# Performance work log

Hardware: AMD Instinct MI355X
Metric: run time of the kernel (lower is better)

## Reference

```python
import jax, jax.numpy as jnp
import numpy as np

NUM_EMBEDDINGS = 1024
EMBEDDING_DIM = 64
COMMITMENT_COST = 0.25


def setup_inputs() -> dict:
    key = jax.random.key(0)
    k1, k2 = jax.random.split(key)
    inputs = jax.random.normal(k1, (32, 4096, EMBEDDING_DIM), dtype=jnp.float32)
    lim = 1.0 / NUM_EMBEDDINGS
    embedding = jax.random.uniform(k2, (NUM_EMBEDDINGS, EMBEDDING_DIM),
                                   dtype=jnp.float32, minval=-lim, maxval=lim)
    return {"inputs": inputs, "embedding": embedding}


def reference(inputs, embedding):
    input_shape = inputs.shape
    flat = inputs.reshape(-1, EMBEDDING_DIM)                     # [N, D]
    # Squared euclidean distances via the expanded form (same math as torch cdist trick)
    distances = (jnp.sum(flat ** 2, axis=1, keepdims=True)
                 + jnp.sum(embedding ** 2, axis=1)
                 - 2.0 * flat @ embedding.T)                     # [N, K]
    encoding_indices = jnp.argmin(distances, axis=1)             # [N]
    # one-hot @ embedding == gather of nearest code rows
    quantized = embedding[encoding_indices].reshape(input_shape)
    e_latent_loss = jnp.mean((jax.lax.stop_gradient(quantized) - inputs) ** 2)
    q_latent_loss = jnp.mean((quantized - jax.lax.stop_gradient(inputs)) ** 2)
    loss = q_latent_loss + COMMITMENT_COST * e_latent_loss
    # straight-through estimator
    quantized_st = inputs + jax.lax.stop_gradient(quantized - inputs)
    return loss, quantized_st, encoding_indices[:, None]
```

## Files before the change

### kernel.cpp

```cpp
#include <hip/hip_runtime.h>

#define D 64
#define K 1024
#define NROWS (32 * 4096)
#define NELEM (NROWS * D)
#define COMMIT 0.25f
#define DELTA 1.2e-4f
#define HDELTA 6e-5f
#define RPB 128
#define CHUNK 128
#define EPAD 68
#define CBYTES (CHUNK * EPAD * 2)

typedef __attribute__((ext_vector_type(8))) short short8v;
typedef __attribute__((ext_vector_type(4))) float f32x4;
typedef unsigned long long u64;

#define FORSLOT8(M) M(0) M(1) M(2) M(3) M(4) M(5) M(6) M(7)

static __device__ __forceinline__ float fence(float v) {
    asm("" : "+v"(v));
    return v;
}

static __device__ __forceinline__ unsigned short f2bf(float f) {
    unsigned u = __float_as_uint(f);
    return (unsigned short)((u + 0x7FFFu + ((u >> 16) & 1u)) >> 16);
}

static __device__ __forceinline__ float np_sumsq64(const float* __restrict__ e) {
    float r[8];
#pragma unroll
    for (int j = 0; j < 8; ++j) r[j] = fence(e[j] * e[j]);
#pragma unroll
    for (int t = 1; t < 8; ++t)
#pragma unroll
        for (int j = 0; j < 8; ++j) r[j] = r[j] + fence(e[8 * t + j] * e[8 * t + j]);
    return ((r[0] + r[1]) + (r[2] + r[3])) + ((r[4] + r[5]) + (r[6] + r[7]));
}

static __device__ __forceinline__ float exact_score(
    const float* __restrict__ xrow, const float* __restrict__ erow, float R,
    float N) {
    float a = 0.0f;
#pragma unroll
    for (int i = 0; i < D; ++i) a = __builtin_fmaf(xrow[i], erow[i], a);
    return (R + N) - 2.0f * a;
}

__global__ void prep_emb_kernel(const float* __restrict__ emb,
                                float* __restrict__ enorm,
                                unsigned short* __restrict__ e_pad,
                                float* __restrict__ loss_slot) {
    int k = blockIdx.x * blockDim.x + threadIdx.x;
    if (k == 0) *loss_slot = 0.0f;
    if (k >= K) return;
    float n = np_sumsq64(emb + k * D);
    enorm[k] = n;
    const float* e = emb + k * D;
    unsigned short* row = e_pad + k * EPAD;
#pragma unroll
    for (int i = 0; i < D; ++i) row[i] = f2bf(e[i]);
    float nh = -0.5f * n;
    unsigned nb = __float_as_uint(nh);
    row[64] = (unsigned short)(nb & 0xFFFFu);
    row[65] = (unsigned short)(nb >> 16);
    row[66] = 0;
    row[67] = 0;
}

#define GLDS(SRC, DST, SZ)                                                  \
    __builtin_amdgcn_global_load_lds(                                       \
        (const __attribute__((address_space(1))) unsigned int*)(SRC),       \
        (__attribute__((address_space(3))) unsigned int*)(DST), SZ, 0, 0)

__global__ __launch_bounds__(256, 1) void argmin_kernel(
    const float* __restrict__ x, const float* __restrict__ emb,
    const float* __restrict__ enorm, const unsigned short* __restrict__ e_pad,
    float* __restrict__ out_q, float* __restrict__ idx_f,
    float* __restrict__ loss_slot) {
    const int tid = threadIdx.x;
    const int l = tid & 63;
    const int w = tid >> 6;
    const int col = l & 15;
    const int koff = (l >> 4) * 8;
    const int blockrow = blockIdx.x * RPB;
    const int wrow = blockrow + w * 32;

    __shared__ unsigned short eB[CHUNK * EPAD];
    __shared__ int cnt[RPB];
    __shared__ int clist[RPB][4];
    __shared__ int bidx[RPB];
    __shared__ float wsum[4];

#define DECL_A(rt, h)                                                       \
    short8v Ahi_##rt##_##h;                                                 \
    { const float* p = x + (size_t)(wrow + rt * 16 + col) * D + h * 32 + koff; \
      float4 q0 = *(const float4*)p, q1 = *(const float4*)(p + 4);          \
      Ahi_##rt##_##h[0] = (short)f2bf(q0.x);                                \
      Ahi_##rt##_##h[1] = (short)f2bf(q0.y);                                \
      Ahi_##rt##_##h[2] = (short)f2bf(q0.z);                                \
      Ahi_##rt##_##h[3] = (short)f2bf(q0.w);                                \
      Ahi_##rt##_##h[4] = (short)f2bf(q1.x);                                \
      Ahi_##rt##_##h[5] = (short)f2bf(q1.y);                                \
      Ahi_##rt##_##h[6] = (short)f2bf(q1.z);                                \
      Ahi_##rt##_##h[7] = (short)f2bf(q1.w); }
    DECL_A(0, 0) DECL_A(0, 1) DECL_A(1, 0) DECL_A(1, 1)

#define SLOTROW(s) (((s) / 4) * 16 + (l >> 4) * 4 + ((s) % 4))

#define STAGE(c)                                                            \
    {                                                                       \
        const char* src = (const char*)e_pad + (size_t)(c) * CBYTES;        \
        char* dst = (char*)eB;                                              \
        _Pragma("unroll")                                                   \
        for (int i = 0; i < 4; ++i) {                                       \
            int off = w * 1024 + i * 4096;                                  \
            GLDS(src + off + l * 16, dst + off, 16);                        \
        }                                                                   \
        { int off4 = 16384 + w * 256;                                       \
          GLDS(src + off4 + l * 4, dst + off4, 4); }                        \
    }

#define DECL_MA(s) float mA_##s = -3.402823466e+38f;
    FORSLOT8(DECL_MA)
#define MFMA2A(rt, sA, sB, sC, sD)                                          \
    { f32x4 acc = {Nc, Nc, Nc, Nc};                                         \
      acc = __builtin_amdgcn_mfma_f32_16x16x32_bf16(Ahi_##rt##_0, Bhi0, acc, 0, 0, 0); \
      acc = __builtin_amdgcn_mfma_f32_16x16x32_bf16(Ahi_##rt##_1, Bhi1, acc, 0, 0, 0); \
      mA_##sA = fmaxf(mA_##sA, acc[0]);                                     \
      mA_##sB = fmaxf(mA_##sB, acc[1]);                                     \
      mA_##sC = fmaxf(mA_##sC, acc[2]);                                     \
      mA_##sD = fmaxf(mA_##sD, acc[3]); }
    for (int c = 0; c < 8; ++c) {
        __syncthreads();
        STAGE(c)
        __syncthreads();
#pragma unroll 2
        for (int nt = 0; nt < 8; ++nt) {
            const int cc = nt * 16 + col;
            const short8v Bhi0 = *(const short8v*)(&eB[cc * EPAD + koff]);
            const short8v Bhi1 = *(const short8v*)(&eB[cc * EPAD + 32 + koff]);
            const float Nc = *(const float*)(&eB[cc * EPAD + 64]);
            MFMA2A(0, 0, 1, 2, 3) MFMA2A(1, 4, 5, 6, 7)
        }
    }
#define BFA(s)                                                              \
    mA_##s = fmaxf(mA_##s, __shfl_xor(mA_##s, 1));                          \
    mA_##s = fmaxf(mA_##s, __shfl_xor(mA_##s, 2));                          \
    mA_##s = fmaxf(mA_##s, __shfl_xor(mA_##s, 4));                          \
    mA_##s = fmaxf(mA_##s, __shfl_xor(mA_##s, 8));
    FORSLOT8(BFA)
#define DECL_T(s) const float thr_##s = mA_##s - HDELTA;
    FORSLOT8(DECL_T)
    if (tid < RPB) cnt[tid] = 0;

#define CHK(s, av)                                                          \
    { if ((av) >= thr_##s) {                                                \
          int row = w * 32 + SLOTROW(s);                                    \
          int pos = atomicAdd(&cnt[row], 1);                                \
          if (pos < 4) clist[row][pos] = code;                              \
      } }
#define MFMA2B(rt, sA, sB, sC, sD)                                          \
    { f32x4 acc = {Nc, Nc, Nc, Nc};                                         \
      acc = __builtin_amdgcn_mfma_f32_16x16x32_bf16(Ahi_##rt##_0, Bhi0, acc, 0, 0, 0); \
      acc = __builtin_amdgcn_mfma_f32_16x16x32_bf16(Ahi_##rt##_1, Bhi1, acc, 0, 0, 0); \
      CHK(sA, acc[0]) CHK(sB, acc[1]) CHK(sC, acc[2]) CHK(sD, acc[3]) }
    for (int c = 0; c < 8; ++c) {
        __syncthreads();
        STAGE(c)
        __syncthreads();
#pragma unroll 2
        for (int nt = 0; nt < 8; ++nt) {
            const int cc = nt * 16 + col;
            const short8v Bhi0 = *(const short8v*)(&eB[cc * EPAD + koff]);
            const short8v Bhi1 = *(const short8v*)(&eB[cc * EPAD + 32 + koff]);
            const float Nc = *(const float*)(&eB[cc * EPAD + 64]);
            const int code = c * CHUNK + cc;
            MFMA2B(0, 0, 1, 2, 3) MFMA2B(1, 4, 5, 6, 7)
        }
    }
    __syncthreads();

    if (tid < RPB) {
        const int row = tid;
        const int n = cnt[row];
        int bk;
        if (n == 1) {
            bk = clist[row][0];
        } else {
            const float* xrow = x + (size_t)(blockrow + row) * D;
            const float R = np_sumsq64(xrow);
            float sb = 3.402823466e+38f;
            int kb = 0x7fffffff;
            if (n <= 4) {
                for (int i = 0; i < n; ++i) {
                    int c = clist[row][i];
                    float s = exact_score(xrow, emb + ((size_t)c << 6), R,
                                          enorm[c]);
                    if (s < sb || (s == sb && c < kb)) { sb = s; kb = c; }
                }
            } else {
                for (int c = 0; c < K; ++c) {
                    float s = exact_score(xrow, emb + ((size_t)c << 6), R,
                                          enorm[c]);
                    if (s < sb || (s == sb && c < kb)) { sb = s; kb = c; }
                }
            }
            bk = kb;
        }
        bidx[row] = bk;
        idx_f[blockrow + row] = (float)bk;
    }
    __syncthreads();

    float lsum = 0.f;
#pragma unroll
    for (int rr = 0; rr < 2; ++rr) {
        const int row = rr * 64 + (tid >> 2);
        const int d0 = (tid & 3) * 16;
        const int bk = bidx[row];
        const float4* xq =
            (const float4*)(x + (size_t)(blockrow + row) * D + d0);
        const float4* eq = (const float4*)(emb + ((size_t)bk << 6) + d0);
        float4* oq = (float4*)(out_q + (size_t)(blockrow + row) * D + d0);
#pragma unroll
        for (int i = 0; i < 4; ++i) {
            float4 xv = xq[i];
            float4 ev = eq[i];
            float dx = ev.x - xv.x, dy = ev.y - xv.y, dz = ev.z - xv.z,
                  dw = ev.w - xv.w;
            float4 o;
            o.x = xv.x + dx;
            o.y = xv.y + dy;
            o.z = xv.z + dz;
            o.w = xv.w + dw;
            oq[i] = o;
            lsum = __builtin_fmaf(dx, dx, lsum);
            lsum = __builtin_fmaf(dy, dy, lsum);
            lsum = __builtin_fmaf(dz, dz, lsum);
            lsum = __builtin_fmaf(dw, dw, lsum);
        }
    }
#pragma unroll
    for (int o = 32; o > 0; o >>= 1) lsum += __shfl_xor(lsum, o);
    if (l == 0) wsum[w] = lsum;
    __syncthreads();
    if (tid == 0)
        atomicAdd(loss_slot, ((wsum[0] + wsum[1]) + (wsum[2] + wsum[3])) *
                                 ((1.0f + COMMIT) / (float)NELEM));
}

extern "C" void kernel_launch(void* const* d_in, const int* in_sizes, int n_in,
                              void* d_out, int out_size, void* d_ws,
                              size_t ws_size, hipStream_t stream) {
    const float* x = (const float*)d_in[0];
    const float* emb = (const float*)d_in[1];

    float* out = (float*)d_out;
    float* loss_slot = out;
    float* out_q = out + 1;
    float* idx_f = out + 1 + NELEM;

    float* enorm = (float*)d_ws;
    unsigned short* e_pad = (unsigned short*)((char*)d_ws + 4096);

    prep_emb_kernel<<<(K + 255) / 256, 256, 0, stream>>>(emb, enorm, e_pad,
                                                         loss_slot);
    argmin_kernel<<<NROWS / RPB, 256, 0, stream>>>(x, emb, enorm, e_pad,
                                                   out_q, idx_f, loss_slot);
}
```

Baseline: 73.50 us.

## Replace two-pass argmin with single-pass running-threshold candidate collection

The old kernel swept the whole codebook twice: first for the per-row max, then again to collect candidates near it. Now a prepass over the first chunk seeds the threshold, and a single sweep collects candidates while tightening the threshold after each chunk. Each block now runs 128 threads, each wave holds 64 rows, and the candidate list holds up to 24 entries. All candidates are always rescored exactly. Early loose thresholds can push more candidates into the list, raising the chance of overflow into the full 1024-code fallback, and fewer waves per block may hurt latency hiding.

```diff
diff --git a/kernel.cpp b/kernel.cpp
--- a/kernel.cpp
+++ b/kernel.cpp
@@ -5,18 +5,20 @@
 #define NROWS (32 * 4096)
 #define NELEM (NROWS * D)
 #define COMMIT 0.25f
-#define DELTA 1.2e-4f
 #define HDELTA 6e-5f
 #define RPB 128
+#define TPB 128
 #define CHUNK 128
 #define EPAD 68
 #define CBYTES (CHUNK * EPAD * 2)
+#define CAP 24
 
 typedef __attribute__((ext_vector_type(8))) short short8v;
 typedef __attribute__((ext_vector_type(4))) float f32x4;
 typedef unsigned long long u64;
 
-#define FORSLOT8(M) M(0) M(1) M(2) M(3) M(4) M(5) M(6) M(7)
+#define FORSLOT(M) M(0) M(1) M(2) M(3) M(4) M(5) M(6) M(7) \
+                   M(8) M(9) M(10) M(11) M(12) M(13) M(14) M(15)
 
 static __device__ __forceinline__ float fence(float v) {
     asm("" : "+v"(v));
@@ -49,14 +51,12 @@
 }
 
 __global__ void prep_emb_kernel(const float* __restrict__ emb,
-                                float* __restrict__ enorm,
                                 unsigned short* __restrict__ e_pad,
                                 float* __restrict__ loss_slot) {
     int k = blockIdx.x * blockDim.x + threadIdx.x;
     if (k == 0) *loss_slot = 0.0f;
     if (k >= K) return;
     float n = np_sumsq64(emb + k * D);
-    enorm[k] = n;
     const float* e = emb + k * D;
     unsigned short* row = e_pad + k * EPAD;
 #pragma unroll
@@ -74,24 +74,23 @@
         (const __attribute__((address_space(1))) unsigned int*)(SRC),       \
         (__attribute__((address_space(3))) unsigned int*)(DST), SZ, 0, 0)
 
-__global__ __launch_bounds__(256, 1) void argmin_kernel(
+__global__ __launch_bounds__(TPB, 1) void argmin_kernel(
     const float* __restrict__ x, const float* __restrict__ emb,
-    const float* __restrict__ enorm, const unsigned short* __restrict__ e_pad,
-    float* __restrict__ out_q, float* __restrict__ idx_f,
-    float* __restrict__ loss_slot) {
+    const unsigned short* __restrict__ e_pad, float* __restrict__ out_q,
+    float* __restrict__ idx_f, float* __restrict__ loss_slot) {
     const int tid = threadIdx.x;
     const int l = tid & 63;
     const int w = tid >> 6;
     const int col = l & 15;
     const int koff = (l >> 4) * 8;
     const int blockrow = blockIdx.x * RPB;
-    const int wrow = blockrow + w * 32;
+    const int wrow = blockrow + w * 64;
 
     __shared__ unsigned short eB[CHUNK * EPAD];
     __shared__ int cnt[RPB];
-    __shared__ int clist[RPB][4];
+    __shared__ unsigned short clist[RPB][CAP];
     __shared__ int bidx[RPB];
-    __shared__ float wsum[4];
+    __shared__ float wsum[2];
 
 #define DECL_A(rt, h)                                                       \
     short8v Ahi_##rt##_##h;                                                 \
@@ -106,25 +105,26 @@
       Ahi_##rt##_##h[6] = (short)f2bf(q1.z);                                \
       Ahi_##rt##_##h[7] = (short)f2bf(q1.w); }
     DECL_A(0, 0) DECL_A(0, 1) DECL_A(1, 0) DECL_A(1, 1)
+    DECL_A(2, 0) DECL_A(2, 1) DECL_A(3, 0) DECL_A(3, 1)
 
 #define SLOTROW(s) (((s) / 4) * 16 + (l >> 4) * 4 + ((s) % 4))
 
 #define STAGE(c)                                                            \
     {                                                                       \
-        const char* src = (const char*)e_pad + (size_t)(c) * CBYTES;        \
-        char* dst = (char*)eB;                                              \
-        _Pragma("unroll")                                                   \
-        for (int i = 0; i < 4; ++i) {                                       \
-            int off = w * 1024 + i * 4096;                                  \
-            GLDS(src + off + l * 16, dst + off, 16);                        \
-        }                                                                   \
-        { int off4 = 16384 + w * 256;                                       \
-          GLDS(src + off4 + l * 4, dst + off4, 4); }                        \
-    }
+        const char* src_ = (const char*)e_pad + (size_t)(c) * CBYTES;       \
+        char* dst_ = (char*)eB;                                             \
+        for (int i_ = w; i_ < 17; i_ += 2)                                  \
+            GLDS(src_ + i_ * 1024 + l * 16, dst_ + i_ * 1024, 16);          \
+    }
+
+    STAGE(0)
+    if (tid < RPB) cnt[tid] = 0;
+    __syncthreads();
 
 #define DECL_MA(s) float mA_##s = -3.402823466e+38f;
-    FORSLOT8(DECL_MA)
-#define MFMA2A(rt, sA, sB, sC, sD)                                          \
+    FORSLOT(DECL_MA)
+
+#define PRM(rt, sA, sB, sC, sD)                                             \
     { f32x4 acc = {Nc, Nc, Nc, Nc};                                         \
       acc = __builtin_amdgcn_mfma_f32_16x16x32_bf16(Ahi_##rt##_0, Bhi0, acc, 0, 0, 0); \
       acc = __builtin_amdgcn_mfma_f32_16x16x32_bf16(Ahi_##rt##_1, Bhi1, acc, 0, 0, 0); \
@@ -132,92 +132,88 @@
       mA_##sB = fmaxf(mA_##sB, acc[1]);                                     \
       mA_##sC = fmaxf(mA_##sC, acc[2]);                                     \
       mA_##sD = fmaxf(mA_##sD, acc[3]); }
+#pragma unroll 2
+    for (int nt = 0; nt < 8; ++nt) {
+        const int cc = nt * 16 + col;
+        const short8v Bhi0 = *(const short8v*)(&eB[cc * EPAD + koff]);
+        const short8v Bhi1 = *(const short8v*)(&eB[cc * EPAD + 32 + koff]);
+        const float Nc = *(const float*)(&eB[cc * EPAD + 64]);
+        PRM(0, 0, 1, 2, 3) PRM(1, 4, 5, 6, 7)
+        PRM(2, 8, 9, 10, 11) PRM(3, 12, 13, 14, 15)
+    }
+#define BFA(s)                                                              \
+    mA_##s = fmaxf(mA_##s, __shfl_xor(mA_##s, 1));                          \
+    mA_##s = fmaxf(mA_##s, __shfl_xor(mA_##s, 2));                          \
+    mA_##s = fmaxf(mA_##s, __shfl_xor(mA_##s, 4));                          \
+    mA_##s = fmaxf(mA_##s, __shfl_xor(mA_##s, 8));
+    FORSLOT(BFA)
+#define DECL_THR(s) float thr_##s = mA_##s - HDELTA;
+    FORSLOT(DECL_THR)
+
+#define CH(s, av)                                                           \
+    { if ((av) >= thr_##s) {                                                \
+          int row_ = w * 64 + SLOTROW(s);                                   \
+          int pos_ = atomicAdd(&cnt[row_], 1);                              \
+          if (pos_ < CAP) clist[row_][pos_] = (unsigned short)code_;        \
+      }                                                                     \
+      mA_##s = fmaxf(mA_##s, (av)); }
+#define COLL(rt, sA, sB, sC, sD)                                            \
+    { f32x4 acc = {Nc, Nc, Nc, Nc};                                         \
+      acc = __builtin_amdgcn_mfma_f32_16x16x32_bf16(Ahi_##rt##_0, Bhi0, acc, 0, 0, 0); \
+      acc = __builtin_amdgcn_mfma_f32_16x16x32_bf16(Ahi_##rt##_1, Bhi1, acc, 0, 0, 0); \
+      CH(sA, acc[0]) CH(sB, acc[1]) CH(sC, acc[2]) CH(sD, acc[3]) }
+#define UPD_THR(s) thr_##s = mA_##s - HDELTA;
     for (int c = 0; c < 8; ++c) {
-        __syncthreads();
-        STAGE(c)
-        __syncthreads();
-#pragma unroll 2
+        if (c > 0) {
+            __syncthreads();
+            STAGE(c)
+            __syncthreads();
+        }
         for (int nt = 0; nt < 8; ++nt) {
             const int cc = nt * 16 + col;
             const short8v Bhi0 = *(const short8v*)(&eB[cc * EPAD + koff]);
             const short8v Bhi1 = *(const short8v*)(&eB[cc * EPAD + 32 + koff]);
             const float Nc = *(const float*)(&eB[cc * EPAD + 64]);
-            MFMA2A(0, 0, 1, 2, 3) MFMA2A(1, 4, 5, 6, 7)
-        }
-    }
-#define BFA(s)                                                              \
-    mA_##s = fmaxf(mA_##s, __shfl_xor(mA_##s, 1));                          \
-    mA_##s = fmaxf(mA_##s, __shfl_xor(mA_##s, 2));                          \
-    mA_##s = fmaxf(mA_##s, __shfl_xor(mA_##s, 4));                          \
-    mA_##s = fmaxf(mA_##s, __shfl_xor(mA_##s, 8));
-    FORSLOT8(BFA)
-#define DECL_T(s) const float thr_##s = mA_##s - HDELTA;
-    FORSLOT8(DECL_T)
-    if (tid < RPB) cnt[tid] = 0;
-
-#define CHK(s, av)                                                          \
-    { if ((av) >= thr_##s) {                                                \
-          int row = w * 32 + SLOTROW(s);                                    \
-          int pos = atomicAdd(&cnt[row], 1);                                \
-          if (pos < 4) clist[row][pos] = code;                              \
-      } }
-#define MFMA2B(rt, sA, sB, sC, sD)                                          \
-    { f32x4 acc = {Nc, Nc, Nc, Nc};                                         \
-      acc = __builtin_amdgcn_mfma_f32_16x16x32_bf16(Ahi_##rt##_0, Bhi0, acc, 0, 0, 0); \
-      acc = __builtin_amdgcn_mfma_f32_16x16x32_bf16(Ahi_##rt##_1, Bhi1, acc, 0, 0, 0); \
-      CHK(sA, acc[0]) CHK(sB, acc[1]) CHK(sC, acc[2]) CHK(sD, acc[3]) }
-    for (int c = 0; c < 8; ++c) {
-        __syncthreads();
-        STAGE(c)
-        __syncthreads();
-#pragma unroll 2
-        for (int nt = 0; nt < 8; ++nt) {
-            const int cc = nt * 16 + col;
-            const short8v Bhi0 = *(const short8v*)(&eB[cc * EPAD + koff]);
-            const short8v Bhi1 = *(const short8v*)(&eB[cc * EPAD + 32 + koff]);
-            const float Nc = *(const float*)(&eB[cc * EPAD + 64]);
-            const int code = c * CHUNK + cc;
-            MFMA2B(0, 0, 1, 2, 3) MFMA2B(1, 4, 5, 6, 7)
-        }
+            const unsigned code_ = (unsigned)(c * CHUNK + cc);
+            COLL(0, 0, 1, 2, 3) COLL(1, 4, 5, 6, 7)
+            COLL(2, 8, 9, 10, 11) COLL(3, 12, 13, 14, 15)
+        }
+        FORSLOT(BFA)
+        FORSLOT(UPD_THR)
     }
     __syncthreads();
 
     if (tid < RPB) {
         const int row = tid;
+        const int grow = blockrow + row;
+        const float* xrow = x + (size_t)grow * D;
+        const float R = np_sumsq64(xrow);
         const int n = cnt[row];
-        int bk;
-        if (n == 1) {
-            bk = clist[row][0];
+        float sb = 3.402823466e+38f;
+        int kb = 0x7fffffff;
+        if (n <= CAP) {
+            for (int i = 0; i < n; ++i) {
+                int c = clist[row][i];
+                float Nk = -2.0f * *(const float*)(&e_pad[c * EPAD + 64]);
+                float s = exact_score(xrow, emb + ((size_t)c << 6), R, Nk);
+                if (s < sb || (s == sb && c < kb)) { sb = s; kb = c; }
+            }
         } else {
-            const float* xrow = x + (size_t)(blockrow + row) * D;
-            const float R = np_sumsq64(xrow);
-            float sb = 3.402823466e+38f;
-            int kb = 0x7fffffff;
-            if (n <= 4) {
-                for (int i = 0; i < n; ++i) {
-                    int c = clist[row][i];
-                    float s = exact_score(xrow, emb + ((size_t)c << 6), R,
-                                          enorm[c]);
-                    if (s < sb || (s == sb && c < kb)) { sb = s; kb = c; }
-                }
-            } else {
-                for (int c = 0; c < K; ++c) {
-                    float s = exact_score(xrow, emb + ((size_t)c << 6), R,
-                                          enorm[c]);
-                    if (s < sb || (s == sb && c < kb)) { sb = s; kb = c; }
-                }
+            for (int c = 0; c < K; ++c) {
+                float Nk = -2.0f * *(const float*)(&e_pad[c * EPAD + 64]);
+                float s = exact_score(xrow, emb + ((size_t)c << 6), R, Nk);
+                if (s < sb || (s == sb && c < kb)) { sb = s; kb = c; }
             }
-            bk = kb;
-        }
-        bidx[row] = bk;
-        idx_f[blockrow + row] = (float)bk;
+        }
+        bidx[row] = kb;
+        idx_f[grow] = (float)kb;
     }
     __syncthreads();
 
     float lsum = 0.f;
 #pragma unroll
-    for (int rr = 0; rr < 2; ++rr) {
-        const int row = rr * 64 + (tid >> 2);
+    for (int rr = 0; rr < 4; ++rr) {
+        const int row = rr * 32 + (tid >> 2);
         const int d0 = (tid & 3) * 16;
         const int bk = bidx[row];
         const float4* xq =
@@ -247,8 +243,8 @@
     if (l == 0) wsum[w] = lsum;
     __syncthreads();
     if (tid == 0)
-        atomicAdd(loss_slot, ((wsum[0] + wsum[1]) + (wsum[2] + wsum[3])) *
-                                 ((1.0f + COMMIT) / (float)NELEM));
+        atomicAdd(loss_slot,
+                  (wsum[0] + wsum[1]) * ((1.0f + COMMIT) / (float)NELEM));
 }
 
 extern "C" void kernel_launch(void* const* d_in, const int* in_sizes, int n_in,
@@ -262,11 +258,10 @@
     float* out_q = out + 1;
     float* idx_f = out + 1 + NELEM;
 
-    float* enorm = (float*)d_ws;
-    unsigned short* e_pad = (unsigned short*)((char*)d_ws + 4096);
-
-    prep_emb_kernel<<<(K + 255) / 256, 256, 0, stream>>>(emb, enorm, e_pad,
+    unsigned short* e_pad = (unsigned short*)d_ws;
+
+    prep_emb_kernel<<<(K + 255) / 256, 256, 0, stream>>>(emb, e_pad,
                                                          loss_slot);
-    argmin_kernel<<<NROWS / RPB, 256, 0, stream>>>(x, emb, enorm, e_pad,
-                                                   out_q, idx_f, loss_slot);
-}
+    argmin_kernel<<<NROWS / RPB, TPB, 0, stream>>>(x, emb, e_pad, out_q,
+                                                   idx_f, loss_slot);
+}
```

Result: slower. 170.9 us (+132.6%).
